# Performance work log

Hardware: AMD Instinct MI355X
Metric: run time of the kernel (lower is better)

The kernel has to match this reference:

```python
import jax, jax.numpy as jnp
import numpy as np

MIDC = 256
HEADS = 8
HEADC = MIDC // HEADS
EPS = 1e-5


def _ln(x, gamma, beta):
    # LayerNorm over last dim (headc)
    mu = jnp.mean(x, axis=-1, keepdims=True)
    var = jnp.var(x, axis=-1, keepdims=True)
    return (x - mu) * jax.lax.rsqrt(var + EPS) * gamma + beta


def setup_inputs() -> dict:
    key = jax.random.key(0)
    ks = jax.random.split(key, 8)
    B, HW, C = 8, 4096, MIDC
    s = 1.0 / np.sqrt(C)
    return {
        "x": jax.random.normal(ks[0], (B, HW, C), jnp.float32),
        "w_qkv": jax.random.normal(ks[1], (C, 3 * C), jnp.float32) * s,
        "b_qkv": jnp.zeros((3 * C,), jnp.float32),
        "kln_g": jnp.ones((HEADC,), jnp.float32),
        "kln_b": jnp.zeros((HEADC,), jnp.float32),
        "vln_g": jnp.ones((HEADC,), jnp.float32),
        "vln_b": jnp.zeros((HEADC,), jnp.float32),
        "w1": jax.random.normal(ks[2], (C, C), jnp.float32) * s,
        "b1": jnp.zeros((C,), jnp.float32),
        "w2": jax.random.normal(ks[3], (C, C), jnp.float32) * s,
        "b2": jnp.zeros((C,), jnp.float32),
    }


def reference(x, w_qkv, b_qkv, kln_g, kln_b, vln_g, vln_b, w1, b1, w2, b2):
    B, HW, C = x.shape
    bias = x
    qkv = (x @ w_qkv + b_qkv).reshape(B, HW, HEADS, 3 * HEADC)
    qkv = qkv.transpose(0, 2, 1, 3)  # [B, h, HW, 3*headc]
    q, k, v = jnp.split(qkv, 3, axis=-1)  # each [B, h, HW, headc]
    k = _ln(k, kln_g, kln_b)
    v = _ln(v, vln_g, vln_b)
    # linear attention: (k^T v)/HW then q @ (.)
    kv = jnp.einsum('bhnd,bhne->bhde', k, v) / HW  # [B, h, headc, headc]
    out = jnp.einsum('bhnd,bhde->bhne', q, kv)     # [B, h, HW, headc]
    out = out.transpose(0, 2, 1, 3).reshape(B, HW, C)
    ret = out + bias
    # GELU MLP (torch nn.GELU default = exact erf form)
    h = jax.nn.gelu(ret @ w1 + b1, approximate=False)
    return h @ w2 + b2 + bias
```

## Files before the change

### kernel.cpp

```cpp
#include <hip/hip_runtime.h>
#include <hip/hip_bf16.h>
#include <math.h>

typedef _Float16 f16;
typedef _Float16 f16x4 __attribute__((ext_vector_type(4)));
typedef _Float16 f16x8 __attribute__((ext_vector_type(8)));
typedef float f32x4 __attribute__((ext_vector_type(4)));

#define MIDC 256
#define NHEADS 8
#define HEADC 32
#define HW_ 4096
#define BATCH 8
#define NTOK (BATCH*HW_)

__device__ __forceinline__ void gload_lds16(const void* g, void* lds){
    __builtin_amdgcn_global_load_lds(
        (const __attribute__((address_space(1))) unsigned int*)g,
        (__attribute__((address_space(3))) unsigned int*)lds, 16, 0, 0);
}

__global__ void k_f32_to_f16(const float* __restrict__ in, f16* __restrict__ out, int n){
    int i = (blockIdx.x*blockDim.x + threadIdx.x)*4;
    if (i < n) {
        float4 v = *reinterpret_cast<const float4*>(in + i);
        f16x4 o = { (f16)v.x, (f16)v.y, (f16)v.z, (f16)v.w };
        *reinterpret_cast<f16x4*>(out + i) = o;
    }
}

__global__ void k_prep(const float* __restrict__ wqkv, const float* __restrict__ w1,
                       const float* __restrict__ w2, const float* __restrict__ bq,
                       f16* __restrict__ wqkvT, f16* __restrict__ w1T,
                       f16* __restrict__ w2T, float* __restrict__ pb){
    int idx = blockIdx.x*blockDim.x + threadIdx.x;
    if (idx < 196608){
        int r = idx / 768, o = idx % 768;
        int h = o / 96, rr = o % 96, p = rr >> 5, d = o & 31;
        int n = (p << 8) + (h << 5) + d;
        wqkvT[(size_t)n*256 + r] = (f16)wqkv[idx];
    } else if (idx < 262144){
        int i = idx - 196608; int r = i >> 8, c = i & 255;
        w1T[(size_t)c*256 + r] = (f16)w1[i];
    } else if (idx < 327680){
        int i = idx - 262144; int r = i >> 8, c = i & 255;
        w2T[(size_t)c*256 + r] = (f16)w2[i];
    } else if (idx < 328448){
        int n = idx - 327680;
        int p = n >> 8, h = (n & 255) >> 5, d = n & 31;
        pb[n] = bq[h*96 + p*32 + d];
    }
}

template<int MODE>
__global__ __launch_bounds__(256) void k_gemm(
    const f16* __restrict__ A, const f16* __restrict__ Bt,
    const float* __restrict__ bias,
    const float* __restrict__ kg_, const float* __restrict__ kb_,
    const float* __restrict__ vg_, const float* __restrict__ vb_,
    f16* __restrict__ oq, f16* __restrict__ ok, f16* __restrict__ ov,
    f16* __restrict__ oh,
    const f16* __restrict__ residh, float* __restrict__ of)
{
    constexpr int K = 256;
    __shared__ __attribute__((aligned(16))) char smem[(MODE==2) ? 32768 : 50176];
    f16* const AsB[2] = { (f16*)(smem),        (f16*)(smem+16384) };
    f16* const BsB[2] = { (f16*)(smem+8192),   (f16*)(smem+24576) };

    const int tid  = threadIdx.x;
    const int lane = tid & 63, wid = tid >> 6;
    const int m0 = blockIdx.y * 128, n0 = blockIdx.x * 128;
    const int wm = (wid >> 1) * 64, wn = (wid & 1) * 64;
    const int lr = lane & 15, kg = lane >> 4;

    f32x4 acc[4][4];
    #pragma unroll
    for (int i=0;i<4;i++)
        #pragma unroll
        for (int j=0;j<4;j++) acc[i][j] = (f32x4){0.f,0.f,0.f,0.f};

    const int srow = tid >> 2, scol = (tid & 3) * 8;
    const f16* gA = A  + (size_t)(m0 + srow)*K + scol;
    const f16* gB = Bt + (size_t)(n0 + srow)*K + scol;
    const size_t rstep = (size_t)64*K;

    auto STAGE = [&](int b, int kt){
        f16* ab = AsB[b] + wid*512;
        f16* bb = BsB[b] + wid*512;
        gload_lds16(gA + kt,          ab);
        gload_lds16(gA + kt + rstep,  ab + 2048);
        gload_lds16(gB + kt,          bb);
        gload_lds16(gB + kt + rstep,  bb + 2048);
    };

    STAGE(1, 0);
    __syncthreads();

    #pragma unroll
    for (int t = 0; t < 8; ++t){
        const f16* Ac = (t & 1) ? AsB[0] : AsB[1];
        const f16* Bc = (t & 1) ? BsB[0] : BsB[1];
        if (t < 7) STAGE((t & 1) ? 1 : 0, (t+1)*32);
        f16x8 a[4], b[4];
        #pragma unroll
        for (int fr=0; fr<4; fr++) a[fr] = *reinterpret_cast<const f16x8*>(Ac + (wm + fr*16 + lr)*32 + kg*8);
        #pragma unroll
        for (int fc=0; fc<4; fc++) b[fc] = *reinterpret_cast<const f16x8*>(Bc + (wn + fc*16 + lr)*32 + kg*8);
        #pragma unroll
        for (int fr=0; fr<4; fr++)
            #pragma unroll
            for (int fc=0; fc<4; fc++)
                acc[fr][fc] = __builtin_amdgcn_mfma_f32_16x16x32_f16(a[fr], b[fc], acc[fr][fc], 0, 0, 0);
        __syncthreads();
    }

    if constexpr (MODE != 2){
        f16* Cs = (f16*)(smem + 16384);
        float bv[4];
        #pragma unroll
        for (int fc=0; fc<4; fc++) bv[fc] = bias[n0 + wn + fc*16 + lr];
        #pragma unroll
        for (int fr=0; fr<4; fr++)
        #pragma unroll
        for (int fc=0; fc<4; fc++)
        #pragma unroll
        for (int r=0; r<4; r++){
            float v = acc[fr][fc][r] + bv[fc];
            if constexpr (MODE == 1) v = 0.5f * v * (1.0f + erff(v * 0.70710678f));
            Cs[(wm + fr*16 + kg*4 + r)*132 + (wn + fc*16 + lr)] = (f16)v;
        }
        __syncthreads();
        #pragma unroll
        for (int i=0;i<2;i++){
            int c = tid + i*256;
            int row = c >> 2, hc = c & 3;
            const f16* src = Cs + row*132 + hc*32;
            f16x8 d0 = *reinterpret_cast<const f16x8*>(src);
            f16x8 d1 = *reinterpret_cast<const f16x8*>(src + 8);
            f16x8 d2 = *reinterpret_cast<const f16x8*>(src + 16);
            f16x8 d3 = *reinterpret_cast<const f16x8*>(src + 24);
            if constexpr (MODE == 0){
                int col0 = n0 + hc*32;
                int part = col0 >> 8;
                int h = (col0 & 255) >> 5;
                int gm = m0 + row, b = gm >> 12, n = gm & 4095;
                f16* dst = (part==0 ? oq : (part==1 ? ok : ov))
                         + ((size_t)(b*NHEADS + h)*HW_ + n)*HEADC;
                if (part == 0){
                    *reinterpret_cast<f16x8*>(dst)      = d0;
                    *reinterpret_cast<f16x8*>(dst + 8)  = d1;
                    *reinterpret_cast<f16x8*>(dst + 16) = d2;
                    *reinterpret_cast<f16x8*>(dst + 24) = d3;
                } else {
                    float vals[32];
                    #pragma unroll
                    for (int j=0;j<8;j++){
                        vals[j]    = (float)d0[j];
                        vals[8+j]  = (float)d1[j];
                        vals[16+j] = (float)d2[j];
                        vals[24+j] = (float)d3[j];
                    }
                    float s = 0.f, s2 = 0.f;
                    #pragma unroll
                    for (int j=0;j<32;j++){ s += vals[j]; s2 = fmaf(vals[j], vals[j], s2); }
                    float mu  = s * (1.0f/32.0f);
                    float var = s2 * (1.0f/32.0f) - mu*mu;
                    float rs  = rsqrtf(var + 1e-5f);
                    const float* gp = (part==1) ? kg_ : vg_;
                    const float* bp = (part==1) ? kb_ : vb_;
                    f16x8 o0, o1, o2, o3;
                    #pragma unroll
                    for (int j=0;j<8;j++){
                        o0[j] = (f16)((vals[j]    - mu)*rs*gp[j]    + bp[j]);
                        o1[j] = (f16)((vals[8+j]  - mu)*rs*gp[8+j]  + bp[8+j]);
                        o2[j] = (f16)((vals[16+j] - mu)*rs*gp[16+j] + bp[16+j]);
                        o3[j] = (f16)((vals[24+j] - mu)*rs*gp[24+j] + bp[24+j]);
                    }
                    *reinterpret_cast<f16x8*>(dst)      = o0;
                    *reinterpret_cast<f16x8*>(dst + 8)  = o1;
                    *reinterpret_cast<f16x8*>(dst + 16) = o2;
                    *reinterpret_cast<f16x8*>(dst + 24) = o3;
                }
            } else {
                f16* dst = oh + (size_t)(m0 + row)*MIDC + n0 + hc*32;
                *reinterpret_cast<f16x8*>(dst)      = d0;
                *reinterpret_cast<f16x8*>(dst + 8)  = d1;
                *reinterpret_cast<f16x8*>(dst + 16) = d2;
                *reinterpret_cast<f16x8*>(dst + 24) = d3;
            }
        }
    } else {
        #pragma unroll
        for (int fr=0; fr<4; fr++)
        #pragma unroll
        for (int fc=0; fc<4; fc++)
        #pragma unroll
        for (int r=0; r<4; r++){
            int gm = m0 + wm + fr*16 + kg*4 + r;
            int gn = n0 + wn + fc*16 + lr;
            size_t xi = (size_t)gm*MIDC + gn;
            of[xi] = acc[fr][fc][r] + bias[gn] + (float)residh[xi];
        }
    }
}

__global__ __launch_bounds__(256) void k_kv(const f16* __restrict__ kb, const f16* __restrict__ vb,
                                            float* __restrict__ kvpart){
    __shared__ __attribute__((aligned(16))) f16 ks[4][64][32];
    __shared__ __attribute__((aligned(16))) f16 vs[4][64][32];
    __shared__ __attribute__((aligned(16))) float red[4][32][32];
    const int bh = blockIdx.x, chunk = blockIdx.y;
    const int tid = threadIdx.x, lane = tid & 63, wid = tid >> 6;
    const int d0 = (lane >> 3) * 4, e0 = (lane & 7) * 4;
    const int tok0 = chunk*256 + wid*64;

    const f16* kg = kb + ((size_t)bh*HW_ + tok0)*HEADC;
    const f16* vg = vb + ((size_t)bh*HW_ + tok0)*HEADC;
    f16* ksw = &ks[wid][0][0]; f16* vsw = &vs[wid][0][0];
    #pragma unroll
    for (int i=0;i<4;i++){
        gload_lds16(kg + (size_t)(i*16 + (lane>>2))*HEADC + (lane&3)*8, ksw + i*512);
        gload_lds16(vg + (size_t)(i*16 + (lane>>2))*HEADC + (lane&3)*8, vsw + i*512);
    }
    __syncthreads();

    f32x4 acc[4];
    #pragma unroll
    for (int i=0;i<4;i++) acc[i] = (f32x4){0.f,0.f,0.f,0.f};
    #pragma unroll 4
    for (int t=0; t<64; t++){
        f16x4 kk = *reinterpret_cast<const f16x4*>(&ks[wid][t][d0]);
        f16x4 vv = *reinterpret_cast<const f16x4*>(&vs[wid][t][e0]);
        f32x4 vf = { (float)vv[0], (float)vv[1], (float)vv[2], (float)vv[3] };
        #pragma unroll
        for (int i=0;i<4;i++) acc[i] += (float)kk[i] * vf;
    }
    __syncthreads();
    #pragma unroll
    for (int i=0;i<4;i++) *reinterpret_cast<f32x4*>(&red[wid][d0+i][e0]) = acc[i];
    __syncthreads();
    int de0 = tid * 4;
    const float* rf = &red[0][0][0];
    f32x4 s = *reinterpret_cast<const f32x4*>(rf + de0);
    #pragma unroll
    for (int w=1; w<4; w++) s += *reinterpret_cast<const f32x4*>(rf + w*1024 + de0);
    *reinterpret_cast<f32x4*>(kvpart + ((size_t)bh*16 + chunk)*1024 + de0) = s;
}

__global__ void k_kvred(const float* __restrict__ kvpart, f16* __restrict__ kvT){
    int gid = blockIdx.x*blockDim.x + threadIdx.x;
    int bh = gid >> 10, de = gid & 1023;
    int d = de >> 5, e = de & 31;
    float s = 0.f;
    #pragma unroll
    for (int p=0; p<16; p++) s += kvpart[((size_t)bh*16 + p)*1024 + de];
    kvT[((size_t)bh << 10) + (e << 5) + d] = (f16)(s * (1.0f/4096.0f));
}

__global__ __launch_bounds__(256) void k_attn(const f16* __restrict__ qb, const f16* __restrict__ kvT,
                                              const f16* __restrict__ xb, f16* __restrict__ ret){
    const int bh = blockIdx.x, chunk = blockIdx.y;
    const int b = bh >> 3, h = bh & 7;
    const int tid = threadIdx.x, lane = tid & 63, wid = tid >> 6;
    const int lr = lane & 15, kg = lane >> 4;
    const int row0 = chunk*128 + wid*32;

    f32x4 acc[2][2];
    #pragma unroll
    for (int i=0;i<2;i++)
        #pragma unroll
        for (int j=0;j<2;j++) acc[i][j] = (f32x4){0.f,0.f,0.f,0.f};

    f16x8 a[2], bb[2];
    #pragma unroll
    for (int fr=0; fr<2; fr++)
        a[fr] = *reinterpret_cast<const f16x8*>(qb + ((size_t)bh*HW_ + row0 + fr*16 + lr)*HEADC + kg*8);
    #pragma unroll
    for (int fc=0; fc<2; fc++)
        bb[fc] = *reinterpret_cast<const f16x8*>(kvT + ((size_t)bh << 10) + (size_t)(fc*16 + lr)*32 + kg*8);
    #pragma unroll
    for (int fr=0; fr<2; fr++)
        #pragma unroll
        for (int fc=0; fc<2; fc++)
            acc[fr][fc] = __builtin_amdgcn_mfma_f32_16x16x32_f16(a[fr], bb[fc], acc[fr][fc], 0, 0, 0);

    #pragma unroll
    for (int fr=0; fr<2; fr++)
    #pragma unroll
    for (int fc=0; fc<2; fc++)
    #pragma unroll
    for (int r=0; r<4; r++){
        int n = row0 + fr*16 + kg*4 + r;
        int e = fc*16 + lr;
        size_t xi = ((size_t)b*HW_ + n)*MIDC + h*HEADC + e;
        ret[xi] = (f16)(acc[fr][fc][r] + (float)xb[xi]);
    }
}

extern "C" void kernel_launch(void* const* d_in, const int* in_sizes, int n_in,
                              void* d_out, int out_size, void* d_ws, size_t ws_size,
                              hipStream_t stream) {
    const float* x     = (const float*)d_in[0];
    const float* w_qkv = (const float*)d_in[1];
    const float* b_qkv = (const float*)d_in[2];
    const float* kln_g = (const float*)d_in[3];
    const float* kln_b = (const float*)d_in[4];
    const float* vln_g = (const float*)d_in[5];
    const float* vln_b = (const float*)d_in[6];
    const float* w1    = (const float*)d_in[7];
    const float* b1    = (const float*)d_in[8];
    const float* w2    = (const float*)d_in[9];
    const float* b2    = (const float*)d_in[10];
    float* out = (float*)d_out;

    char* ws = (char*)d_ws;
    size_t off = 0;
    auto alloc = [&](size_t bytes) -> void* {
        void* p = ws + off; off += (bytes + 255) & ~255ULL; return p;
    };
    const size_t TOKB = (size_t)NTOK*MIDC*sizeof(f16);
    f16* xb    = (f16*)alloc(TOKB);
    f16* wqkvT = (f16*)alloc(768*256*sizeof(f16));
    f16* w1T   = (f16*)alloc(256*256*sizeof(f16));
    f16* w2T   = (f16*)alloc(256*256*sizeof(f16));
    float* pb  = (float*)alloc(768*sizeof(float));
    f16* qb    = (f16*)alloc(TOKB);
    f16* kb    = (f16*)alloc(TOKB);
    f16* vb    = (f16*)alloc(TOKB);
    float* kvpart = (float*)alloc((size_t)64*16*1024*sizeof(float));
    f16* kvT   = (f16*)alloc((size_t)64*1024*sizeof(f16));
    f16* retb = vb;
    f16* hb   = kb;

    k_f32_to_f16<<<dim3((NTOK*MIDC)/4/256), 256, 0, stream>>>(x, xb, NTOK*MIDC);
    k_prep<<<dim3((328448+255)/256), 256, 0, stream>>>(w_qkv, w1, w2, b_qkv, wqkvT, w1T, w2T, pb);

    k_gemm<0><<<dim3(768/128, NTOK/128), 256, 0, stream>>>(
        xb, wqkvT, pb, kln_g, kln_b, vln_g, vln_b,
        qb, kb, vb, nullptr, nullptr, nullptr);

    k_kv<<<dim3(64, HW_/256), 256, 0, stream>>>(kb, vb, kvpart);
    k_kvred<<<dim3(65536/256), 256, 0, stream>>>(kvpart, kvT);

    k_attn<<<dim3(64, HW_/128), 256, 0, stream>>>(qb, kvT, xb, retb);

    k_gemm<1><<<dim3(256/128, NTOK/128), 256, 0, stream>>>(
        retb, w1T, b1, nullptr, nullptr, nullptr, nullptr,
        nullptr, nullptr, nullptr, hb, nullptr, nullptr);

    k_gemm<2><<<dim3(256/128, NTOK/128), 256, 0, stream>>>(
        hb, w2T, b2, nullptr, nullptr, nullptr, nullptr,
        nullptr, nullptr, nullptr, nullptr, xb, out);
}
```

Before: 211.8 us.

## Enlarge GEMM tiles to 256x128 with 512 threads and XCD-aware block remap

The GEMM kernel now uses 512-thread blocks computing 256x128 output tiles, so each staged B tile is shared by twice as many rows of A and B global traffic drops. Block indices are remapped so consecutive workgroups are spread across the 8 XCDs for better L2 locality. The epilogue writes through LDS in two halves because the staging buffer only holds 128 rows. Costs are larger shared memory per block, fewer blocks in flight, and an extra barrier in the epilogue.

```diff
diff --git a/kernel.cpp b/kernel.cpp
--- a/kernel.cpp
+++ b/kernel.cpp
@@ -52,8 +52,8 @@
     }
 }
 
-template<int MODE>
-__global__ __launch_bounds__(256) void k_gemm(
+template<int MODE, int GX>
+__global__ __launch_bounds__(512, 4) void k_gemm(
     const f16* __restrict__ A, const f16* __restrict__ Bt,
     const float* __restrict__ bias,
     const float* __restrict__ kg_, const float* __restrict__ kb_,
@@ -63,14 +63,19 @@
     const f16* __restrict__ residh, float* __restrict__ of)
 {
     constexpr int K = 256;
-    __shared__ __attribute__((aligned(16))) char smem[(MODE==2) ? 32768 : 50176];
-    f16* const AsB[2] = { (f16*)(smem),        (f16*)(smem+16384) };
-    f16* const BsB[2] = { (f16*)(smem+8192),   (f16*)(smem+24576) };
+    __shared__ __attribute__((aligned(16))) char smem[49152];
 
     const int tid  = threadIdx.x;
     const int lane = tid & 63, wid = tid >> 6;
-    const int m0 = blockIdx.y * 128, n0 = blockIdx.x * 128;
-    const int wm = (wid >> 1) * 64, wn = (wid & 1) * 64;
+
+    const int nwg  = GX * (NTOK/256);
+    const int orig = blockIdx.x + GX*blockIdx.y;
+    const int lin  = (orig & 7) * (nwg >> 3) + (orig >> 3);
+    const int bx = lin % GX, by = lin / GX;
+    const int m0 = by * 256, n0 = bx * 128;
+
+    const int wm = (wid >> 1) * 64;
+    const int wn = (wid & 1) * 64;
     const int lr = lane & 15, kg = lane >> 4;
 
     f32x4 acc[4][4];
@@ -82,68 +87,74 @@
     const int srow = tid >> 2, scol = (tid & 3) * 8;
     const f16* gA = A  + (size_t)(m0 + srow)*K + scol;
     const f16* gB = Bt + (size_t)(n0 + srow)*K + scol;
-    const size_t rstep = (size_t)64*K;
 
     auto STAGE = [&](int b, int kt){
-        f16* ab = AsB[b] + wid*512;
-        f16* bb = BsB[b] + wid*512;
-        gload_lds16(gA + kt,          ab);
-        gload_lds16(gA + kt + rstep,  ab + 2048);
-        gload_lds16(gB + kt,          bb);
-        gload_lds16(gB + kt + rstep,  bb + 2048);
+        f16* base = (f16*)(smem + b*24576);
+        f16* ab = base + wid*512;
+        f16* bb = base + 8192 + wid*512;
+        gload_lds16(gA + kt,                  ab);
+        gload_lds16(gA + kt + (size_t)128*K,  ab + 4096);
+        gload_lds16(gB + kt,                  bb);
     };
-
-    STAGE(1, 0);
-    __syncthreads();
-
-    #pragma unroll
-    for (int t = 0; t < 8; ++t){
-        const f16* Ac = (t & 1) ? AsB[0] : AsB[1];
-        const f16* Bc = (t & 1) ? BsB[0] : BsB[1];
-        if (t < 7) STAGE((t & 1) ? 1 : 0, (t+1)*32);
-        f16x8 a[4], b[4];
-        #pragma unroll
-        for (int fr=0; fr<4; fr++) a[fr] = *reinterpret_cast<const f16x8*>(Ac + (wm + fr*16 + lr)*32 + kg*8);
-        #pragma unroll
-        for (int fc=0; fc<4; fc++) b[fc] = *reinterpret_cast<const f16x8*>(Bc + (wn + fc*16 + lr)*32 + kg*8);
+    auto COMPUTE = [&](int b){
+        const f16* base = (const f16*)(smem + b*24576);
+        const f16* Bf = base + 8192;
+        f16x8 a[4], bf[4];
+        #pragma unroll
+        for (int fr=0; fr<4; fr++) a[fr]  = *reinterpret_cast<const f16x8*>(base + (wm + fr*16 + lr)*32 + kg*8);
+        #pragma unroll
+        for (int fc=0; fc<4; fc++) bf[fc] = *reinterpret_cast<const f16x8*>(Bf + (wn + fc*16 + lr)*32 + kg*8);
         #pragma unroll
         for (int fr=0; fr<4; fr++)
             #pragma unroll
             for (int fc=0; fc<4; fc++)
-                acc[fr][fc] = __builtin_amdgcn_mfma_f32_16x16x32_f16(a[fr], b[fc], acc[fr][fc], 0, 0, 0);
+                acc[fr][fc] = __builtin_amdgcn_mfma_f32_16x16x32_f16(a[fr], bf[fc], acc[fr][fc], 0, 0, 0);
+    };
+
+    STAGE(0, 0);
+    __syncthreads();
+    #pragma unroll
+    for (int t = 0; t < 8; ++t){
+        const int cur = t & 1;
+        if (t < 7) STAGE(cur ^ 1, (t+1)*32);
+        COMPUTE(cur);
         __syncthreads();
     }
 
     if constexpr (MODE != 2){
-        f16* Cs = (f16*)(smem + 16384);
+        f16* Cs = (f16*)smem;
         float bv[4];
         #pragma unroll
         for (int fc=0; fc<4; fc++) bv[fc] = bias[n0 + wn + fc*16 + lr];
         #pragma unroll
-        for (int fr=0; fr<4; fr++)
-        #pragma unroll
-        for (int fc=0; fc<4; fc++)
-        #pragma unroll
-        for (int r=0; r<4; r++){
-            float v = acc[fr][fc][r] + bv[fc];
-            if constexpr (MODE == 1) v = 0.5f * v * (1.0f + erff(v * 0.70710678f));
-            Cs[(wm + fr*16 + kg*4 + r)*132 + (wn + fc*16 + lr)] = (f16)v;
-        }
-        __syncthreads();
-        #pragma unroll
-        for (int i=0;i<2;i++){
-            int c = tid + i*256;
-            int row = c >> 2, hc = c & 3;
+        for (int half=0; half<2; ++half){
+            if (half) __syncthreads();
+            if ((wid >> 2) == half){
+                int rbase = wm - half*128;
+                #pragma unroll
+                for (int fr=0; fr<4; fr++)
+                #pragma unroll
+                for (int fc=0; fc<4; fc++)
+                #pragma unroll
+                for (int r=0; r<4; r++){
+                    float v = acc[fr][fc][r] + bv[fc];
+                    if constexpr (MODE == 1) v = 0.5f * v * (1.0f + erff(v * 0.70710678f));
+                    Cs[(rbase + fr*16 + kg*4 + r)*132 + (wn + fc*16 + lr)] = (f16)v;
+                }
+            }
+            __syncthreads();
+            int row = tid >> 2, hc = tid & 3;
             const f16* src = Cs + row*132 + hc*32;
             f16x8 d0 = *reinterpret_cast<const f16x8*>(src);
             f16x8 d1 = *reinterpret_cast<const f16x8*>(src + 8);
             f16x8 d2 = *reinterpret_cast<const f16x8*>(src + 16);
             f16x8 d3 = *reinterpret_cast<const f16x8*>(src + 24);
+            int gm = m0 + half*128 + row;
             if constexpr (MODE == 0){
                 int col0 = n0 + hc*32;
                 int part = col0 >> 8;
                 int h = (col0 & 255) >> 5;
-                int gm = m0 + row, b = gm >> 12, n = gm & 4095;
+                int b = gm >> 12, n = gm & 4095;
                 f16* dst = (part==0 ? oq : (part==1 ? ok : ov))
                          + ((size_t)(b*NHEADS + h)*HW_ + n)*HEADC;
                 if (part == 0){
@@ -182,7 +193,7 @@
                     *reinterpret_cast<f16x8*>(dst + 24) = o3;
                 }
             } else {
-                f16* dst = oh + (size_t)(m0 + row)*MIDC + n0 + hc*32;
+                f16* dst = oh + (size_t)gm*MIDC + n0 + hc*32;
                 *reinterpret_cast<f16x8*>(dst)      = d0;
                 *reinterpret_cast<f16x8*>(dst + 8)  = d1;
                 *reinterpret_cast<f16x8*>(dst + 16) = d2;
@@ -335,7 +346,7 @@
     k_f32_to_f16<<<dim3((NTOK*MIDC)/4/256), 256, 0, stream>>>(x, xb, NTOK*MIDC);
     k_prep<<<dim3((328448+255)/256), 256, 0, stream>>>(w_qkv, w1, w2, b_qkv, wqkvT, w1T, w2T, pb);
 
-    k_gemm<0><<<dim3(768/128, NTOK/128), 256, 0, stream>>>(
+    k_gemm<0,6><<<dim3(6, NTOK/256), 512, 0, stream>>>(
         xb, wqkvT, pb, kln_g, kln_b, vln_g, vln_b,
         qb, kb, vb, nullptr, nullptr, nullptr);
 
@@ -344,11 +355,11 @@
 
     k_attn<<<dim3(64, HW_/128), 256, 0, stream>>>(qb, kvT, xb, retb);
 
-    k_gemm<1><<<dim3(256/128, NTOK/128), 256, 0, stream>>>(
+    k_gemm<1,2><<<dim3(2, NTOK/256), 512, 0, stream>>>(
         retb, w1T, b1, nullptr, nullptr, nullptr, nullptr,
         nullptr, nullptr, nullptr, hb, nullptr, nullptr);
 
-    k_gemm<2><<<dim3(256/128, NTOK/128), 256, 0, stream>>>(
+    k_gemm<2,2><<<dim3(2, NTOK/256), 512, 0, stream>>>(
         hb, w2T, b2, nullptr, nullptr, nullptr, nullptr,
         nullptr, nullptr, nullptr, nullptr, xb, out);
 }
```

New measurement: 255.7 us. 1.21x slower.

## Split GEMM into QKV and MLP kernels with smaller tiles and block swizzle

Applied to the files above, without the earlier changes.

Splits the templated GEMM into a QKV kernel and an MLP kernel. The MLP kernel uses 128x64 tiles, less shared memory and a launch bound of four blocks per CU, giving more workgroups and higher occupancy for the N=256 GEMMs. Both kernels remap block indices with a swizzle meant to improve L2 locality. The attention epilogue now stages results through LDS so the residual add can use vectorized, coalesced loads and stores instead of scattered scalar accesses. Smaller MLP tiles reload A twice as often, which adds memory traffic.

```diff
diff --git a/kernel.cpp b/kernel.cpp
--- a/kernel.cpp
+++ b/kernel.cpp
@@ -52,24 +52,27 @@
     }
 }
 
-template<int MODE>
-__global__ __launch_bounds__(256) void k_gemm(
+__global__ __launch_bounds__(256) void k_gemm0(
     const f16* __restrict__ A, const f16* __restrict__ Bt,
     const float* __restrict__ bias,
     const float* __restrict__ kg_, const float* __restrict__ kb_,
     const float* __restrict__ vg_, const float* __restrict__ vb_,
-    f16* __restrict__ oq, f16* __restrict__ ok, f16* __restrict__ ov,
-    f16* __restrict__ oh,
-    const f16* __restrict__ residh, float* __restrict__ of)
+    f16* __restrict__ oq, f16* __restrict__ ok, f16* __restrict__ ov)
 {
     constexpr int K = 256;
-    __shared__ __attribute__((aligned(16))) char smem[(MODE==2) ? 32768 : 50176];
+    __shared__ __attribute__((aligned(16))) char smem[50176];
     f16* const AsB[2] = { (f16*)(smem),        (f16*)(smem+16384) };
     f16* const BsB[2] = { (f16*)(smem+8192),   (f16*)(smem+24576) };
 
     const int tid  = threadIdx.x;
     const int lane = tid & 63, wid = tid >> 6;
-    const int m0 = blockIdx.y * 128, n0 = blockIdx.x * 128;
+
+    const int nwg  = 6 * 256;
+    const int orig = blockIdx.x + 6*blockIdx.y;
+    const int lin  = (orig & 7) * (nwg >> 3) + (orig >> 3);
+    const int bx = lin % 6, by = lin / 6;
+    const int m0 = by * 128, n0 = bx * 128;
+
     const int wm = (wid >> 1) * 64, wn = (wid & 1) * 64;
     const int lr = lane & 15, kg = lane >> 4;
 
@@ -93,14 +96,14 @@
         gload_lds16(gB + kt + rstep,  bb + 2048);
     };
 
-    STAGE(1, 0);
-    __syncthreads();
-
+    STAGE(0, 0);
+    __syncthreads();
     #pragma unroll
     for (int t = 0; t < 8; ++t){
-        const f16* Ac = (t & 1) ? AsB[0] : AsB[1];
-        const f16* Bc = (t & 1) ? BsB[0] : BsB[1];
-        if (t < 7) STAGE((t & 1) ? 1 : 0, (t+1)*32);
+        const int cur = t & 1;
+        if (t < 7) STAGE(cur ^ 1, (t+1)*32);
+        const f16* Ac = AsB[cur];
+        const f16* Bc = BsB[cur];
         f16x8 a[4], b[4];
         #pragma unroll
         for (int fr=0; fr<4; fr++) a[fr] = *reinterpret_cast<const f16x8*>(Ac + (wm + fr*16 + lr)*32 + kg*8);
@@ -114,92 +117,174 @@
         __syncthreads();
     }
 
-    if constexpr (MODE != 2){
-        f16* Cs = (f16*)(smem + 16384);
-        float bv[4];
-        #pragma unroll
-        for (int fc=0; fc<4; fc++) bv[fc] = bias[n0 + wn + fc*16 + lr];
+    f16* Cs = (f16*)(smem + 16384);
+    float bv[4];
+    #pragma unroll
+    for (int fc=0; fc<4; fc++) bv[fc] = bias[n0 + wn + fc*16 + lr];
+    #pragma unroll
+    for (int fr=0; fr<4; fr++)
+    #pragma unroll
+    for (int fc=0; fc<4; fc++)
+    #pragma unroll
+    for (int r=0; r<4; r++){
+        float v = acc[fr][fc][r] + bv[fc];
+        Cs[(wm + fr*16 + kg*4 + r)*132 + (wn + fc*16 + lr)] = (f16)v;
+    }
+    __syncthreads();
+    int part = n0 >> 8;
+    #pragma unroll
+    for (int i=0;i<2;i++){
+        int c = tid + i*256;
+        int row = c >> 2, hc = c & 3;
+        const f16* src = Cs + row*132 + hc*32;
+        f16x8 d0 = *reinterpret_cast<const f16x8*>(src);
+        f16x8 d1 = *reinterpret_cast<const f16x8*>(src + 8);
+        f16x8 d2 = *reinterpret_cast<const f16x8*>(src + 16);
+        f16x8 d3 = *reinterpret_cast<const f16x8*>(src + 24);
+        int col0 = n0 + hc*32;
+        int h = (col0 & 255) >> 5;
+        int gm = m0 + row, b = gm >> 12, n = gm & 4095;
+        f16* dst = (part==0 ? oq : (part==1 ? ok : ov))
+                 + ((size_t)(b*NHEADS + h)*HW_ + n)*HEADC;
+        if (part == 0){
+            *reinterpret_cast<f16x8*>(dst)      = d0;
+            *reinterpret_cast<f16x8*>(dst + 8)  = d1;
+            *reinterpret_cast<f16x8*>(dst + 16) = d2;
+            *reinterpret_cast<f16x8*>(dst + 24) = d3;
+        } else {
+            float vals[32];
+            #pragma unroll
+            for (int j=0;j<8;j++){
+                vals[j]    = (float)d0[j];
+                vals[8+j]  = (float)d1[j];
+                vals[16+j] = (float)d2[j];
+                vals[24+j] = (float)d3[j];
+            }
+            float s = 0.f, s2 = 0.f;
+            #pragma unroll
+            for (int j=0;j<32;j++){ s += vals[j]; s2 = fmaf(vals[j], vals[j], s2); }
+            float mu  = s * (1.0f/32.0f);
+            float var = s2 * (1.0f/32.0f) - mu*mu;
+            float rs  = rsqrtf(var + 1e-5f);
+            const float* gp = (part==1) ? kg_ : vg_;
+            const float* bp = (part==1) ? kb_ : vb_;
+            f16x8 o0, o1, o2, o3;
+            #pragma unroll
+            for (int j=0;j<8;j++){
+                o0[j] = (f16)((vals[j]    - mu)*rs*gp[j]    + bp[j]);
+                o1[j] = (f16)((vals[8+j]  - mu)*rs*gp[8+j]  + bp[8+j]);
+                o2[j] = (f16)((vals[16+j] - mu)*rs*gp[16+j] + bp[16+j]);
+                o3[j] = (f16)((vals[24+j] - mu)*rs*gp[24+j] + bp[24+j]);
+            }
+            *reinterpret_cast<f16x8*>(dst)      = o0;
+            *reinterpret_cast<f16x8*>(dst + 8)  = o1;
+            *reinterpret_cast<f16x8*>(dst + 16) = o2;
+            *reinterpret_cast<f16x8*>(dst + 24) = o3;
+        }
+    }
+}
+
+template<int MODE>
+__global__ __launch_bounds__(256, 4) void k_mlp(
+    const f16* __restrict__ A, const f16* __restrict__ Bt,
+    const float* __restrict__ bias,
+    f16* __restrict__ oh,
+    const f16* __restrict__ residh, float* __restrict__ of)
+{
+    constexpr int K = 256;
+    __shared__ __attribute__((aligned(16))) char smem[24576];
+
+    const int tid  = threadIdx.x;
+    const int lane = tid & 63, wid = tid >> 6;
+
+    const int nwg  = 4 * 256;
+    const int orig = blockIdx.x + 4*blockIdx.y;
+    const int lin  = (orig & 7) * (nwg >> 3) + (orig >> 3);
+    const int bx = lin & 3, by = lin >> 2;
+    const int m0 = by * 128, n0 = bx * 64;
+
+    const int wm = (wid >> 1) * 64;
+    const int wn = (wid & 1) * 32;
+    const int lr = lane & 15, kg = lane >> 4;
+
+    f32x4 acc[4][2];
+    #pragma unroll
+    for (int i=0;i<4;i++)
+        #pragma unroll
+        for (int j=0;j<2;j++) acc[i][j] = (f32x4){0.f,0.f,0.f,0.f};
+
+    const int srow = tid >> 2, scol = (tid & 3) * 8;
+    const f16* gA = A  + (size_t)(m0 + srow)*K + scol;
+    const f16* gB = Bt + (size_t)(n0 + srow)*K + scol;
+
+    auto STAGE = [&](int b, int kt){
+        f16* Ab = (f16*)(smem + b*12288);
+        f16* Bb = Ab + 4096;
+        gload_lds16(gA + kt,                 Ab + wid*512);
+        gload_lds16(gA + kt + (size_t)64*K,  Ab + 2048 + wid*512);
+        gload_lds16(gB + kt,                 Bb + wid*512);
+    };
+
+    STAGE(0, 0);
+    __syncthreads();
+    #pragma unroll
+    for (int t = 0; t < 8; ++t){
+        const int cur = t & 1;
+        if (t < 7) STAGE(cur ^ 1, (t+1)*32);
+        const f16* Ab = (const f16*)(smem + cur*12288);
+        const f16* Bb = Ab + 4096;
+        f16x8 a[4], bf[2];
+        #pragma unroll
+        for (int fr=0; fr<4; fr++) a[fr]  = *reinterpret_cast<const f16x8*>(Ab + (wm + fr*16 + lr)*32 + kg*8);
+        #pragma unroll
+        for (int fc=0; fc<2; fc++) bf[fc] = *reinterpret_cast<const f16x8*>(Bb + (wn + fc*16 + lr)*32 + kg*8);
         #pragma unroll
         for (int fr=0; fr<4; fr++)
-        #pragma unroll
-        for (int fc=0; fc<4; fc++)
+            #pragma unroll
+            for (int fc=0; fc<2; fc++)
+                acc[fr][fc] = __builtin_amdgcn_mfma_f32_16x16x32_f16(a[fr], bf[fc], acc[fr][fc], 0, 0, 0);
+        __syncthreads();
+    }
+
+    float bv[2];
+    #pragma unroll
+    for (int fc=0; fc<2; fc++) bv[fc] = bias[n0 + wn + fc*16 + lr];
+
+    if constexpr (MODE == 1){
+        f16* Cs = (f16*)smem;
+        #pragma unroll
+        for (int fr=0; fr<4; fr++)
+        #pragma unroll
+        for (int fc=0; fc<2; fc++)
         #pragma unroll
         for (int r=0; r<4; r++){
             float v = acc[fr][fc][r] + bv[fc];
-            if constexpr (MODE == 1) v = 0.5f * v * (1.0f + erff(v * 0.70710678f));
-            Cs[(wm + fr*16 + kg*4 + r)*132 + (wn + fc*16 + lr)] = (f16)v;
+            v = 0.5f * v * (1.0f + erff(v * 0.70710678f));
+            Cs[(wm + fr*16 + kg*4 + r)*72 + (wn + fc*16 + lr)] = (f16)v;
         }
         __syncthreads();
-        #pragma unroll
-        for (int i=0;i<2;i++){
-            int c = tid + i*256;
-            int row = c >> 2, hc = c & 3;
-            const f16* src = Cs + row*132 + hc*32;
-            f16x8 d0 = *reinterpret_cast<const f16x8*>(src);
-            f16x8 d1 = *reinterpret_cast<const f16x8*>(src + 8);
-            f16x8 d2 = *reinterpret_cast<const f16x8*>(src + 16);
-            f16x8 d3 = *reinterpret_cast<const f16x8*>(src + 24);
-            if constexpr (MODE == 0){
-                int col0 = n0 + hc*32;
-                int part = col0 >> 8;
-                int h = (col0 & 255) >> 5;
-                int gm = m0 + row, b = gm >> 12, n = gm & 4095;
-                f16* dst = (part==0 ? oq : (part==1 ? ok : ov))
-                         + ((size_t)(b*NHEADS + h)*HW_ + n)*HEADC;
-                if (part == 0){
-                    *reinterpret_cast<f16x8*>(dst)      = d0;
-                    *reinterpret_cast<f16x8*>(dst + 8)  = d1;
-                    *reinterpret_cast<f16x8*>(dst + 16) = d2;
-                    *reinterpret_cast<f16x8*>(dst + 24) = d3;
-                } else {
-                    float vals[32];
-                    #pragma unroll
-                    for (int j=0;j<8;j++){
-                        vals[j]    = (float)d0[j];
-                        vals[8+j]  = (float)d1[j];
-                        vals[16+j] = (float)d2[j];
-                        vals[24+j] = (float)d3[j];
-                    }
-                    float s = 0.f, s2 = 0.f;
-                    #pragma unroll
-                    for (int j=0;j<32;j++){ s += vals[j]; s2 = fmaf(vals[j], vals[j], s2); }
-                    float mu  = s * (1.0f/32.0f);
-                    float var = s2 * (1.0f/32.0f) - mu*mu;
-                    float rs  = rsqrtf(var + 1e-5f);
-                    const float* gp = (part==1) ? kg_ : vg_;
-                    const float* bp = (part==1) ? kb_ : vb_;
-                    f16x8 o0, o1, o2, o3;
-                    #pragma unroll
-                    for (int j=0;j<8;j++){
-                        o0[j] = (f16)((vals[j]    - mu)*rs*gp[j]    + bp[j]);
-                        o1[j] = (f16)((vals[8+j]  - mu)*rs*gp[8+j]  + bp[8+j]);
-                        o2[j] = (f16)((vals[16+j] - mu)*rs*gp[16+j] + bp[16+j]);
-                        o3[j] = (f16)((vals[24+j] - mu)*rs*gp[24+j] + bp[24+j]);
-                    }
-                    *reinterpret_cast<f16x8*>(dst)      = o0;
-                    *reinterpret_cast<f16x8*>(dst + 8)  = o1;
-                    *reinterpret_cast<f16x8*>(dst + 16) = o2;
-                    *reinterpret_cast<f16x8*>(dst + 24) = o3;
-                }
-            } else {
-                f16* dst = oh + (size_t)(m0 + row)*MIDC + n0 + hc*32;
-                *reinterpret_cast<f16x8*>(dst)      = d0;
-                *reinterpret_cast<f16x8*>(dst + 8)  = d1;
-                *reinterpret_cast<f16x8*>(dst + 16) = d2;
-                *reinterpret_cast<f16x8*>(dst + 24) = d3;
-            }
-        }
+        int row = tid >> 1, ch = tid & 1;
+        const f16* src = Cs + row*72 + ch*32;
+        f16x8 d0 = *reinterpret_cast<const f16x8*>(src);
+        f16x8 d1 = *reinterpret_cast<const f16x8*>(src + 8);
+        f16x8 d2 = *reinterpret_cast<const f16x8*>(src + 16);
+        f16x8 d3 = *reinterpret_cast<const f16x8*>(src + 24);
+        f16* dst = oh + (size_t)(m0 + row)*MIDC + n0 + ch*32;
+        *reinterpret_cast<f16x8*>(dst)      = d0;
+        *reinterpret_cast<f16x8*>(dst + 8)  = d1;
+        *reinterpret_cast<f16x8*>(dst + 16) = d2;
+        *reinterpret_cast<f16x8*>(dst + 24) = d3;
     } else {
         #pragma unroll
         for (int fr=0; fr<4; fr++)
         #pragma unroll
-        for (int fc=0; fc<4; fc++)
+        for (int fc=0; fc<2; fc++)
         #pragma unroll
         for (int r=0; r<4; r++){
             int gm = m0 + wm + fr*16 + kg*4 + r;
             int gn = n0 + wn + fc*16 + lr;
             size_t xi = (size_t)gm*MIDC + gn;
-            of[xi] = acc[fr][fc][r] + bias[gn] + (float)residh[xi];
+            of[xi] = acc[fr][fc][r] + bv[fc] + (float)residh[xi];
         }
     }
 }
@@ -259,6 +344,7 @@
 
 __global__ __launch_bounds__(256) void k_attn(const f16* __restrict__ qb, const f16* __restrict__ kvT,
                                               const f16* __restrict__ xb, f16* __restrict__ ret){
+    __shared__ __attribute__((aligned(16))) f16 Ls[128][40];
     const int bh = blockIdx.x, chunk = blockIdx.y;
     const int b = bh >> 3, h = bh & 7;
     const int tid = threadIdx.x, lane = tid & 63, wid = tid >> 6;
@@ -289,12 +375,24 @@
     #pragma unroll
     for (int fc=0; fc<2; fc++)
     #pragma unroll
-    for (int r=0; r<4; r++){
-        int n = row0 + fr*16 + kg*4 + r;
-        int e = fc*16 + lr;
-        size_t xi = ((size_t)b*HW_ + n)*MIDC + h*HEADC + e;
-        ret[xi] = (f16)(acc[fr][fc][r] + (float)xb[xi]);
-    }
+    for (int r=0; r<4; r++)
+        Ls[wid*32 + fr*16 + kg*4 + r][fc*16 + lr] = (f16)acc[fr][fc][r];
+    __syncthreads();
+
+    int row = tid >> 1, hf = tid & 1;
+    size_t base = ((size_t)b*HW_ + chunk*128 + row)*MIDC + h*HEADC + hf*16;
+    f16x8 x0 = *reinterpret_cast<const f16x8*>(xb + base);
+    f16x8 x1 = *reinterpret_cast<const f16x8*>(xb + base + 8);
+    f16x8 s0 = *reinterpret_cast<const f16x8*>(&Ls[row][hf*16]);
+    f16x8 s1 = *reinterpret_cast<const f16x8*>(&Ls[row][hf*16 + 8]);
+    f16x8 o0, o1;
+    #pragma unroll
+    for (int j=0;j<8;j++){
+        o0[j] = (f16)((float)s0[j] + (float)x0[j]);
+        o1[j] = (f16)((float)s1[j] + (float)x1[j]);
+    }
+    *reinterpret_cast<f16x8*>(ret + base)     = o0;
+    *reinterpret_cast<f16x8*>(ret + base + 8) = o1;
 }
 
 extern "C" void kernel_launch(void* const* d_in, const int* in_sizes, int n_in,
@@ -335,20 +433,17 @@
     k_f32_to_f16<<<dim3((NTOK*MIDC)/4/256), 256, 0, stream>>>(x, xb, NTOK*MIDC);
     k_prep<<<dim3((328448+255)/256), 256, 0, stream>>>(w_qkv, w1, w2, b_qkv, wqkvT, w1T, w2T, pb);
 
-    k_gemm<0><<<dim3(768/128, NTOK/128), 256, 0, stream>>>(
-        xb, wqkvT, pb, kln_g, kln_b, vln_g, vln_b,
-        qb, kb, vb, nullptr, nullptr, nullptr);
+    k_gemm0<<<dim3(6, NTOK/128), 256, 0, stream>>>(
+        xb, wqkvT, pb, kln_g, kln_b, vln_g, vln_b, qb, kb, vb);
 
     k_kv<<<dim3(64, HW_/256), 256, 0, stream>>>(kb, vb, kvpart);
     k_kvred<<<dim3(65536/256), 256, 0, stream>>>(kvpart, kvT);
 
     k_attn<<<dim3(64, HW_/128), 256, 0, stream>>>(qb, kvT, xb, retb);
 
-    k_gemm<1><<<dim3(256/128, NTOK/128), 256, 0, stream>>>(
-        retb, w1T, b1, nullptr, nullptr, nullptr, nullptr,
-        nullptr, nullptr, nullptr, hb, nullptr, nullptr);
-
-    k_gemm<2><<<dim3(256/128, NTOK/128), 256, 0, stream>>>(
-        hb, w2T, b2, nullptr, nullptr, nullptr, nullptr,
-        nullptr, nullptr, nullptr, nullptr, xb, out);
-}
+    k_mlp<1><<<dim3(4, NTOK/128), 256, 0, stream>>>(
+        retb, w1T, b1, hb, nullptr, nullptr);
+
+    k_mlp<2><<<dim3(4, NTOK/128), 256, 0, stream>>>(
+        hb, w2T, b2, nullptr, xb, out);
+}
```

Result: faster. 200.0 us (-5.6%).
